# Kernel tuning notes

Measured on AMD Instinct MI355X. Metric: run time of the kernel, lower is better.

The kernel has to match this reference:

```python
import jax, jax.numpy as jnp
import numpy as np

B, C, H, W = 4, 64, 64, 64  # prompt and kv share the same BCHW shape
EPS = 1e-5
OFR = 4.0  # offset_range_factor
SCALE = (C // 1) ** -0.5  # n_head_channels = dim / n_heads = 64


def conv1x1(x, w, b=None):
    y = jnp.einsum('oc,bchw->bohw', w, x)
    if b is not None:
        y = y + b[None, :, None, None]
    return y


def grid_sample_bilinear(img, grid):
    # img: [N,C,Hp,Wp], grid: [N,Hg,Wg,2] with (x,y) in [-1,1], align_corners=True, zeros padding
    N, Cc, Hp, Wp = img.shape
    Hg, Wg = grid.shape[1], grid.shape[2]
    gx = (grid[..., 0] + 1.0) * 0.5 * (Wp - 1)
    gy = (grid[..., 1] + 1.0) * 0.5 * (Hp - 1)
    x0 = jnp.floor(gx)
    y0 = jnp.floor(gy)
    img_f = img.reshape(N, Cc, Hp * Wp)

    def gather(xi, yi):
        valid = (xi >= 0) & (xi <= Wp - 1) & (yi >= 0) & (yi <= Hp - 1)
        xi_c = jnp.clip(xi, 0, Wp - 1).astype(jnp.int32)
        yi_c = jnp.clip(yi, 0, Hp - 1).astype(jnp.int32)
        idx = (yi_c * Wp + xi_c).reshape(N, 1, -1)
        vals = jnp.take_along_axis(img_f, idx, axis=2)  # [N,C,Hg*Wg]
        return vals, valid.reshape(N, 1, -1).astype(img.dtype)

    v00, m00 = gather(x0, y0)
    v01, m01 = gather(x0 + 1, y0)
    v10, m10 = gather(x0, y0 + 1)
    v11, m11 = gather(x0 + 1, y0 + 1)
    wx = (gx - x0).reshape(N, 1, -1)
    wy = (gy - y0).reshape(N, 1, -1)
    out = (v00 * m00 * (1 - wx) * (1 - wy) + v01 * m01 * wx * (1 - wy)
           + v10 * m10 * (1 - wx) * wy + v11 * m11 * wx * wy)
    return out.reshape(N, Cc, Hg, Wg)


def setup_inputs() -> dict:
    key = jax.random.key(0)
    ks = jax.random.split(key, 8)
    s = 0.02
    return {
        'prompt': jax.random.normal(ks[0], (B, C, H, W), jnp.float32),
        'kv': jax.random.normal(ks[1], (B, C, H, W), jnp.float32),
        'wq': s * jax.random.normal(ks[2], (C, C), jnp.float32),
        'bq': jnp.zeros((C,), jnp.float32),
        'wk': s * jax.random.normal(ks[3], (C, C), jnp.float32),
        'bk': jnp.zeros((C,), jnp.float32),
        'wv': s * jax.random.normal(ks[4], (C, C), jnp.float32),
        'bv': jnp.zeros((C,), jnp.float32),
        'wo': s * jax.random.normal(ks[5], (C, C), jnp.float32),
        'bo': jnp.zeros((C,), jnp.float32),
        'dw_w': s * jax.random.normal(ks[6], (C, 1, 3, 3), jnp.float32),  # depthwise 3x3
        'dw_b': jnp.zeros((C,), jnp.float32),
        'ln_w': jnp.ones((C,), jnp.float32),
        'ln_b': jnp.zeros((C,), jnp.float32),
        'off_w': s * jax.random.normal(ks[7], (2, C), jnp.float32),  # 1x1 conv to 2 offset channels
    }


def reference(prompt, kv, wq, bq, wk, bk, wv, bv, wo, bo, dw_w, dw_b, ln_w, ln_b, off_w):
    # q projection (n_groups=1 so group view == full view)
    q = conv1x1(prompt, wq, bq)  # [B,C,H,W]

    # conv_offset: depthwise 3x3 -> WithBias LayerNorm over channels -> GELU -> 1x1 to 2ch
    t = jax.lax.conv_general_dilated(q, dw_w, (1, 1), ((1, 1), (1, 1)),
                                     feature_group_count=C)
    t = t + dw_b[None, :, None, None]
    mu = t.mean(axis=1, keepdims=True)
    var = t.var(axis=1, keepdims=True)
    t = (t - mu) / jnp.sqrt(var + EPS) * ln_w[None, :, None, None] + ln_b[None, :, None, None]
    t = jax.nn.gelu(t, approximate=False)
    offset = jnp.einsum('oc,bchw->bohw', off_w, t)  # [B,2,H,W] (y,x) channels

    Hk, Wk = offset.shape[2], offset.shape[3]
    n = Hk * Wk
    rng = jnp.array([1.0 / (Hk - 1.0), 1.0 / (Wk - 1.0)], dtype=offset.dtype).reshape(1, 2, 1, 1)
    offset = jnp.tanh(offset) * rng * OFR
    offset = jnp.transpose(offset, (0, 2, 3, 1))  # [B,Hk,Wk,2] (y,x)

    ref_y = (jnp.linspace(0.5, Hk - 0.5, Hk) / (Hk - 1.0)) * 2.0 - 1.0
    ref_x = (jnp.linspace(0.5, Wk - 0.5, Wk) / (Wk - 1.0)) * 2.0 - 1.0
    ry, rx = jnp.meshgrid(ref_y, ref_x, indexing='ij')
    ref = jnp.stack((ry, rx), axis=-1)[None].astype(offset.dtype)  # [1,Hk,Wk,2]

    pos = offset + ref
    grid = pos[..., ::-1]  # swap to (x,y)
    xs = grid_sample_bilinear(kv, grid)  # [B,C,Hk,Wk]
    xs = xs.reshape(B, C, n)

    k = jnp.einsum('oc,bcn->bon', wk, xs) + bk[None, :, None]
    v = jnp.einsum('oc,bcn->bon', wv, xs) + bv[None, :, None]
    qf = q.reshape(B, C, H * W)

    attn = jnp.einsum('bcm,bcn->bmn', qf, k) * SCALE  # [B,HW,n]
    attn = jax.nn.softmax(attn, axis=2)
    out = jnp.einsum('bmn,bcn->bcm', attn, v).reshape(B, C, H, W)
    return conv1x1(out, wo, bo)
```

## Files before the change

kernel.cpp:

```cpp
#include <hip/hip_runtime.h>
#include <math.h>

#define BB 4
#define CC 64
#define HH 64
#define WW 64
#define HWP 4096
#define NPTS 4096
#define LDP 72
constexpr float K_EPS   = 1e-5f;
constexpr float K_OFR   = 4.0f;
constexpr float K_QSCALE = 0.18033688011112042f;


typedef short frag8 __attribute__((ext_vector_type(8)));
typedef float f32x4 __attribute__((ext_vector_type(4)));

static __device__ inline unsigned short f2bf(float f) {
  unsigned int u = __builtin_bit_cast(unsigned int, f);
  unsigned int r = (u + 0x7fffu + ((u >> 16) & 1u)) >> 16;
  return (unsigned short)r;
}

__global__ __launch_bounds__(512) void k_qproj(
    const float* __restrict__ prompt, const float* __restrict__ wq,
    const float* __restrict__ bq, float* __restrict__ qf,
    unsigned short* __restrict__ qb) {
  __shared__ float w_s[64 * 64];
  __shared__ float p_s[64 * 64];
  __shared__ unsigned short t_s[64 * 68];
  int tid = threadIdx.x;
  int blk = blockIdx.x;
  int b = blk >> 6; int hw0 = (blk & 63) * 64;
#pragma unroll
  for (int i = 0; i < 8; ++i) w_s[i * 512 + tid] = wq[i * 512 + tid];
#pragma unroll
  for (int i = 0; i < 8; ++i) {
    int idx = i * 512 + tid; int c = idx >> 6, pix = idx & 63;
    p_s[idx] = prompt[(size_t)(b * CC + c) * HWP + hw0 + pix];
  }
  __syncthreads();
  int x = tid & 63, og = tid >> 6;
  float acc[8];
#pragma unroll
  for (int oo = 0; oo < 8; ++oo) acc[oo] = bq[og * 8 + oo];
  for (int cg = 0; cg < 16; ++cg) {
    float p0 = p_s[(cg * 4 + 0) * 64 + x];
    float p1 = p_s[(cg * 4 + 1) * 64 + x];
    float p2 = p_s[(cg * 4 + 2) * 64 + x];
    float p3 = p_s[(cg * 4 + 3) * 64 + x];
#pragma unroll
    for (int oo = 0; oo < 8; ++oo) {
      const float4 w4 = *(const float4*)&w_s[(og * 8 + oo) * 64 + cg * 4];
      acc[oo] = fmaf(w4.x, p0, fmaf(w4.y, p1, fmaf(w4.z, p2, fmaf(w4.w, p3, acc[oo]))));
    }
  }
#pragma unroll
  for (int oo = 0; oo < 8; ++oo) {
    int o = og * 8 + oo;
    qf[(size_t)(b * CC + o) * HWP + hw0 + x] = acc[oo];
    t_s[x * 68 + o] = f2bf(acc[oo] * K_QSCALE);
  }
  __syncthreads();
#pragma unroll
  for (int i = 0; i < 2; ++i) {
    int idx = i * 512 + tid;
    int pix = idx >> 4, c4 = idx & 15;
    ushort4 v = *(const ushort4*)&t_s[pix * 68 + c4 * 4];
    *(ushort4*)&qb[(size_t)(b * HWP + hw0 + pix) * CC + c4 * 4] = v;
  }
}

__global__ __launch_bounds__(512) void k_off_sample(
    const float* __restrict__ q, const float* __restrict__ dw_w,
    const float* __restrict__ dw_b, const float* __restrict__ ln_w,
    const float* __restrict__ ln_b, const float* __restrict__ off_w,
    const float* __restrict__ kv,
    const float* __restrict__ wk, const float* __restrict__ bk,
    const float* __restrict__ wv, const float* __restrict__ bv,
    unsigned short* __restrict__ kb, unsigned short* __restrict__ vb) {
  __shared__ float wk_s[64 * 64];
  __shared__ float wv_s[64 * 64];
  __shared__ float xs_s[64 * 64];
  __shared__ float red0[8][64];
  __shared__ float red1[8][64];

  int tid = threadIdx.x;
  int x = tid & 63;
  int cg = tid >> 6;
  int by = blockIdx.x;
  int b = by >> 6;
  int y = by & 63;

#pragma unroll
  for (int i = 0; i < 8; ++i) {
    wk_s[i * 512 + tid] = wk[i * 512 + tid];
    wv_s[i * 512 + tid] = wv[i * 512 + tid];
  }

  float t[8];
#pragma unroll
  for (int i = 0; i < 8; ++i) {
    int c = cg * 8 + i;
    float acc = dw_b[c];
    const float* qc = q + (size_t)(b * CC + c) * HWP;
#pragma unroll
    for (int ky = 0; ky < 3; ++ky) {
      int yy = y + ky - 1;
      bool yok = (yy >= 0) && (yy < HH);
#pragma unroll
      for (int kx = 0; kx < 3; ++kx) {
        int xx = x + kx - 1;
        bool ok = yok && (xx >= 0) && (xx < WW);
        float v = ok ? qc[yy * WW + xx] : 0.f;
        acc = fmaf(dw_w[c * 9 + ky * 3 + kx], v, acc);
      }
    }
    t[i] = acc;
  }
  float s1 = 0.f, s2 = 0.f;
#pragma unroll
  for (int i = 0; i < 8; ++i) { s1 += t[i]; s2 += t[i] * t[i]; }
  red0[cg][x] = s1;
  red1[cg][x] = s2;
  __syncthreads();
  float mu = 0.f, ms = 0.f;
#pragma unroll
  for (int g = 0; g < 8; ++g) { mu += red0[g][x]; ms += red1[g][x]; }
  mu *= (1.f / 64.f); ms *= (1.f / 64.f);
  float rstd = rsqrtf(ms - mu * mu + K_EPS);

  float oy = 0.f, ox = 0.f;
#pragma unroll
  for (int i = 0; i < 8; ++i) {
    int c = cg * 8 + i;
    float g = (t[i] - mu) * rstd * ln_w[c] + ln_b[c];
    g = 0.5f * g * (1.f + erff(g * 0.70710678118654752f));
    oy = fmaf(off_w[c], g, oy);
    ox = fmaf(off_w[CC + c], g, ox);
  }
  __syncthreads();
  red0[cg][x] = oy;
  red1[cg][x] = ox;
  __syncthreads();
  if (cg == 0) {
    float osy = 0.f, osx = 0.f;
#pragma unroll
    for (int g = 0; g < 8; ++g) { osy += red0[g][x]; osx += red1[g][x]; }
    osy = tanhf(osy) * (K_OFR / (HH - 1));
    osx = tanhf(osx) * (K_OFR / (WW - 1));
    float ry = (y + 0.5f) * (2.f / 63.f) - 1.f;
    float rx = (x + 0.5f) * (2.f / 63.f) - 1.f;
    red0[0][x] = (osx + rx + 1.f) * 0.5f * (WW - 1);
    red0[1][x] = (osy + ry + 1.f) * 0.5f * (HH - 1);
  }
  __syncthreads();

  int n = x, og = cg;
  int n0 = y * 64;
  float gx = red0[0][n], gy = red0[1][n];
  float x0f = floorf(gx), y0f = floorf(gy);
  float wx = gx - x0f, wy = gy - y0f;
  int x0 = (int)x0f, y0 = (int)y0f;
  int x1 = x0 + 1, y1 = y0 + 1;
  float m00 = (x0 >= 0 && x0 < WW && y0 >= 0 && y0 < HH) ? 1.f : 0.f;
  float m01 = (x1 >= 0 && x1 < WW && y0 >= 0 && y0 < HH) ? 1.f : 0.f;
  float m10 = (x0 >= 0 && x0 < WW && y1 >= 0 && y1 < HH) ? 1.f : 0.f;
  float m11 = (x1 >= 0 && x1 < WW && y1 >= 0 && y1 < HH) ? 1.f : 0.f;
  int x0c = min(max(x0, 0), WW - 1), x1c = min(max(x1, 0), WW - 1);
  int y0c = min(max(y0, 0), HH - 1), y1c = min(max(y1, 0), HH - 1);
  int i00 = y0c * WW + x0c, i01 = y0c * WW + x1c;
  int i10 = y1c * WW + x0c, i11 = y1c * WW + x1c;
  float w00 = m00 * (1.f - wx) * (1.f - wy);
  float w01 = m01 * wx * (1.f - wy);
  float w10 = m10 * (1.f - wx) * wy;
  float w11 = m11 * wx * wy;

  const float* base = kv + (size_t)b * CC * HWP;
#pragma unroll
  for (int i = 0; i < 8; ++i) {
    int c = og * 8 + i;
    const float* pc = base + (size_t)c * HWP;
    xs_s[c * 64 + n] = w00 * pc[i00] + w01 * pc[i01] + w10 * pc[i10] + w11 * pc[i11];
  }
  __syncthreads();
  float ak[8], av[8];
#pragma unroll
  for (int oo = 0; oo < 8; ++oo) { ak[oo] = bk[og * 8 + oo]; av[oo] = bv[og * 8 + oo]; }
  for (int cg2 = 0; cg2 < 16; ++cg2) {
    float p0 = xs_s[(cg2 * 4 + 0) * 64 + n];
    float p1 = xs_s[(cg2 * 4 + 1) * 64 + n];
    float p2 = xs_s[(cg2 * 4 + 2) * 64 + n];
    float p3 = xs_s[(cg2 * 4 + 3) * 64 + n];
#pragma unroll
    for (int oo = 0; oo < 8; ++oo) {
      int o = og * 8 + oo;
      const float4 k4 = *(const float4*)&wk_s[o * 64 + cg2 * 4];
      const float4 v4 = *(const float4*)&wv_s[o * 64 + cg2 * 4];
      ak[oo] = fmaf(k4.x, p0, fmaf(k4.y, p1, fmaf(k4.z, p2, fmaf(k4.w, p3, ak[oo]))));
      av[oo] = fmaf(v4.x, p0, fmaf(v4.y, p1, fmaf(v4.z, p2, fmaf(v4.w, p3, av[oo]))));
    }
  }
  unsigned short tk[8];
#pragma unroll
  for (int oo = 0; oo < 8; ++oo) tk[oo] = f2bf(ak[oo]);
  size_t krow = (size_t)(b * NPTS + n0 + n) * CC + og * 8;
  *(uint4*)&kb[krow] = *(const uint4*)&tk[0];
#pragma unroll
  for (int oo = 0; oo < 8; ++oo) {
    int o = og * 8 + oo;
    vb[(size_t)(b * CC + o) * NPTS + n0 + n] = f2bf(av[oo]);
  }
}

__global__ __launch_bounds__(256) void k_attn(
    const unsigned short* __restrict__ qb, const unsigned short* __restrict__ kb,
    const unsigned short* __restrict__ vb, float* __restrict__ opart,
    float* __restrict__ dpart, int ns_shift) {
  __shared__ short qp_s[64 * LDP];
  __shared__ short k_s[64 * LDP];
  __shared__ short v_s[64 * LDP];

  int tid = threadIdx.x;
  int w = tid >> 6, lane = tid & 63, quad = lane >> 4, l16 = lane & 15;
  int blk = blockIdx.x;
  int mt = blk & 63; int bns = blk >> 6;
  int ns = bns & ((1 << ns_shift) - 1); int b = bns >> ns_shift;
  int m0 = mt * 64;

  const unsigned short* qbb = qb + (size_t)b * HWP * CC;
  const unsigned short* kbb = kb + (size_t)b * NPTS * CC;
  const unsigned short* vbb = vb + (size_t)b * CC * NPTS;

#pragma unroll
  for (int pass = 0; pass < 2; ++pass) {
    int idx = pass * 256 + tid;
    int row = idx >> 3, part = idx & 7;
    uint4 d = *(const uint4*)(qbb + (size_t)(m0 + row) * CC + part * 8);
    *(uint4*)&qp_s[row * LDP + part * 8] = d;
  }
  __syncthreads();
  frag8 a_frag[2];
#pragma unroll
  for (int kc = 0; kc < 2; ++kc)
    a_frag[kc] = *(const frag8*)&qp_s[(w * 16 + l16) * LDP + kc * 32 + quad * 8];

  f32x4 o_acc[4];
  float d_acc[4];
#pragma unroll
  for (int i = 0; i < 4; ++i) {
    d_acc[i] = 0.f;
    o_acc[i][0] = 0.f; o_acc[i][1] = 0.f; o_acc[i][2] = 0.f; o_acc[i][3] = 0.f;
  }

  int niters = (NPTS / 64) >> ns_shift;
  int nbase = ns * niters * 64;
  for (int it = 0; it < niters; ++it) {
    int n0 = nbase + it * 64;
    __syncthreads();
#pragma unroll
    for (int pass = 0; pass < 2; ++pass) {
      int idx = pass * 256 + tid;
      int row = idx >> 3, part = idx & 7;
      uint4 dk = *(const uint4*)(kbb + (size_t)(n0 + row) * CC + part * 8);
      uint4 dv = *(const uint4*)(vbb + (size_t)row * NPTS + n0 + part * 8);
      *(uint4*)&k_s[row * LDP + part * 8] = dk;
      *(uint4*)&v_s[row * LDP + part * 8] = dv;
    }
    __syncthreads();

    f32x4 s_acc[4];
#pragma unroll
    for (int t = 0; t < 4; ++t) {
      s_acc[t][0] = 0.f; s_acc[t][1] = 0.f; s_acc[t][2] = 0.f; s_acc[t][3] = 0.f;
    }
#pragma unroll
    for (int kc = 0; kc < 2; ++kc) {
#pragma unroll
      for (int t = 0; t < 4; ++t) {
        frag8 bf = *(const frag8*)&k_s[(t * 16 + l16) * LDP + kc * 32 + quad * 8];
        s_acc[t] = __builtin_amdgcn_mfma_f32_16x16x32_bf16(a_frag[kc], bf, s_acc[t], 0, 0, 0);
      }
    }
#pragma unroll
    for (int t = 0; t < 4; ++t) {
#pragma unroll
      for (int r = 0; r < 4; ++r) {
        float pv = exp2f(s_acc[t][r]);
        unsigned short ph = f2bf(pv);
        qp_s[(w * 16 + quad * 4 + r) * LDP + t * 16 + l16] = (short)ph;
        d_acc[r] += __builtin_bit_cast(float, (unsigned int)ph << 16);
      }
    }
#pragma unroll
    for (int kc = 0; kc < 2; ++kc) {
      frag8 bp = *(const frag8*)&qp_s[(w * 16 + l16) * LDP + kc * 32 + quad * 8];
#pragma unroll
      for (int ct = 0; ct < 4; ++ct) {
        frag8 av = *(const frag8*)&v_s[(ct * 16 + l16) * LDP + kc * 32 + quad * 8];
        o_acc[ct] = __builtin_amdgcn_mfma_f32_16x16x32_bf16(av, bp, o_acc[ct], 0, 0, 0);
      }
    }
  }

  float* op = opart + (size_t)((ns * BB + b) * HWP + m0 + w * 16 + l16) * CC;
#pragma unroll
  for (int ct = 0; ct < 4; ++ct) {
    float4 o4;
    o4.x = o_acc[ct][0]; o4.y = o_acc[ct][1]; o4.z = o_acc[ct][2]; o4.w = o_acc[ct][3];
    *(float4*)&op[ct * 16 + quad * 4] = o4;
  }
#pragma unroll
  for (int r = 0; r < 4; ++r) {
    float d = d_acc[r];
    d += __shfl_xor(d, 1); d += __shfl_xor(d, 2);
    d += __shfl_xor(d, 4); d += __shfl_xor(d, 8);
    if (l16 == 0)
      dpart[(ns * BB + b) * HWP + m0 + w * 16 + quad * 4 + r] = d;
  }
}

__global__ __launch_bounds__(256) void k_out(
    const float* __restrict__ opart, const float* __restrict__ dpart,
    const float* __restrict__ wo, const float* __restrict__ bo,
    float* __restrict__ out, int NS) {
  __shared__ float wo_s[CC * CC];
  __shared__ float t_s[64 * 65];
  int tid = threadIdx.x;
  int blk = blockIdx.x;
  int b = blk >> 6, mt = blk & 63, m0 = mt * 64;
  for (int i = tid; i < CC * CC; i += 256) wo_s[i] = wo[i];

#pragma unroll
  for (int it = 0; it < 16; ++it) {
    int idx = it * 256 + tid;
    int m = idx >> 6, c = idx & 63;
    float o = 0.f, d = 0.f;
    for (int s = 0; s < NS; ++s) {
      o += opart[(size_t)((s * BB + b) * HWP + m0 + m) * CC + c];
      d += dpart[(s * BB + b) * HWP + m0 + m];
    }
    t_s[m * 65 + c] = o / d;
  }
  __syncthreads();
  int ml = tid & 63, og = tid >> 6;
  for (int oo = 0; oo < 16; ++oo) {
    int o = og * 16 + oo;
    float acc = bo[o];
#pragma unroll
    for (int c = 0; c < 64; ++c) acc = fmaf(wo_s[o * CC + c], t_s[ml * 65 + c], acc);
    out[(size_t)(b * CC + o) * HWP + m0 + ml] = acc;
  }
}

extern "C" void kernel_launch(void* const* d_in, const int* in_sizes, int n_in,
                              void* d_out, int out_size, void* d_ws, size_t ws_size,
                              hipStream_t stream) {
  const float* prompt = (const float*)d_in[0];
  const float* kv     = (const float*)d_in[1];
  const float* wq     = (const float*)d_in[2];
  const float* bq     = (const float*)d_in[3];
  const float* wk     = (const float*)d_in[4];
  const float* bk     = (const float*)d_in[5];
  const float* wv     = (const float*)d_in[6];
  const float* bv     = (const float*)d_in[7];
  const float* wo     = (const float*)d_in[8];
  const float* bo     = (const float*)d_in[9];
  const float* dw_w   = (const float*)d_in[10];
  const float* dw_b   = (const float*)d_in[11];
  const float* ln_w   = (const float*)d_in[12];
  const float* ln_b   = (const float*)d_in[13];
  const float* off_w  = (const float*)d_in[14];
  float* out = (float*)d_out;
  float* ws  = (float*)d_ws;

  const size_t need4 = (size_t)(4 * 1048576 + 3 * 524288 + 4 * 16384) * sizeof(float);
  int NS, ns_shift;
  if (ws_size >= need4) { NS = 4; ns_shift = 2; } else { NS = 2; ns_shift = 1; }

  float* opart          = ws;
  float* qf             = ws;
  unsigned short* qb    = (unsigned short*)(ws + (size_t)NS * 1048576);
  unsigned short* kb    = (unsigned short*)(ws + (size_t)NS * 1048576 + 524288);
  unsigned short* vb    = (unsigned short*)(ws + (size_t)NS * 1048576 + 2 * 524288);
  float* dpart          = ws + (size_t)NS * 1048576 + 3 * 524288;

  hipLaunchKernelGGL(k_qproj, dim3(BB * 64), dim3(512), 0, stream,
                     prompt, wq, bq, qf, qb);
  hipLaunchKernelGGL(k_off_sample, dim3(BB * HH), dim3(512), 0, stream,
                     qf, dw_w, dw_b, ln_w, ln_b, off_w,
                     kv, wk, bk, wv, bv, kb, vb);
  hipLaunchKernelGGL(k_attn, dim3(BB * NS * 64), dim3(256), 0, stream,
                     qb, kb, vb, opart, dpart, ns_shift);
  hipLaunchKernelGGL(k_out, dim3(BB * 64), dim3(256), 0, stream,
                     opart, dpart, wo, bo, out, NS);
}
```

Before: 177.7 us.

## Widen blocks, compute softmax denominator via MFMA, packed bf16 exp, more key splits

Several changes land at once. The projection and offset kernels move to 1024-thread blocks. The attention kernel computes S transposed so each lane holds contiguous columns, which it writes as packed bf16 pairs using native exp2 and pack conversion. The row-sum denominator now comes from an MFMA against a vector of ones instead of shuffle reductions. The key dimension is split into 8 when workspace allows, attention blocks are reordered so one query tile's key splits run adjacently, and the output kernel uses smaller tiles. Together these aim to raise parallelism and cut VALU and shuffle work, at the cost of more partial-sum traffic in the output kernel.

```diff
diff --git a/kernel.cpp b/kernel.cpp
--- a/kernel.cpp
+++ b/kernel.cpp
@@ -22,7 +22,28 @@
   return (unsigned short)r;
 }
 
-__global__ __launch_bounds__(512) void k_qproj(
+#if defined(__has_builtin)
+#if __has_builtin(__builtin_amdgcn_cvt_pk_bf16_f32)
+#define HAVE_CVT_PK_BF16 1
+#endif
+#if __has_builtin(__builtin_amdgcn_exp2f)
+#define EXP2F(x) __builtin_amdgcn_exp2f(x)
+#endif
+#endif
+#ifndef EXP2F
+#define EXP2F(x) exp2f(x)
+#endif
+
+static __device__ inline int pack2bf(float a, float b) {
+#ifdef HAVE_CVT_PK_BF16
+  auto r = __builtin_amdgcn_cvt_pk_bf16_f32(a, b);
+  return __builtin_bit_cast(int, r);
+#else
+  return (int)f2bf(a) | ((int)f2bf(b) << 16);
+#endif
+}
+
+__global__ __launch_bounds__(1024) void k_qproj(
     const float* __restrict__ prompt, const float* __restrict__ wq,
     const float* __restrict__ bq, float* __restrict__ qf,
     unsigned short* __restrict__ qb) {
@@ -33,45 +54,43 @@
   int blk = blockIdx.x;
   int b = blk >> 6; int hw0 = (blk & 63) * 64;
 #pragma unroll
-  for (int i = 0; i < 8; ++i) w_s[i * 512 + tid] = wq[i * 512 + tid];
-#pragma unroll
-  for (int i = 0; i < 8; ++i) {
-    int idx = i * 512 + tid; int c = idx >> 6, pix = idx & 63;
+  for (int i = 0; i < 4; ++i) w_s[i * 1024 + tid] = wq[i * 1024 + tid];
+#pragma unroll
+  for (int i = 0; i < 4; ++i) {
+    int idx = i * 1024 + tid; int c = idx >> 6, pix = idx & 63;
     p_s[idx] = prompt[(size_t)(b * CC + c) * HWP + hw0 + pix];
   }
   __syncthreads();
   int x = tid & 63, og = tid >> 6;
-  float acc[8];
-#pragma unroll
-  for (int oo = 0; oo < 8; ++oo) acc[oo] = bq[og * 8 + oo];
+  float acc[4];
+#pragma unroll
+  for (int oo = 0; oo < 4; ++oo) acc[oo] = bq[og * 4 + oo];
   for (int cg = 0; cg < 16; ++cg) {
     float p0 = p_s[(cg * 4 + 0) * 64 + x];
     float p1 = p_s[(cg * 4 + 1) * 64 + x];
     float p2 = p_s[(cg * 4 + 2) * 64 + x];
     float p3 = p_s[(cg * 4 + 3) * 64 + x];
 #pragma unroll
-    for (int oo = 0; oo < 8; ++oo) {
-      const float4 w4 = *(const float4*)&w_s[(og * 8 + oo) * 64 + cg * 4];
+    for (int oo = 0; oo < 4; ++oo) {
+      const float4 w4 = *(const float4*)&w_s[(og * 4 + oo) * 64 + cg * 4];
       acc[oo] = fmaf(w4.x, p0, fmaf(w4.y, p1, fmaf(w4.z, p2, fmaf(w4.w, p3, acc[oo]))));
     }
   }
 #pragma unroll
-  for (int oo = 0; oo < 8; ++oo) {
-    int o = og * 8 + oo;
+  for (int oo = 0; oo < 4; ++oo) {
+    int o = og * 4 + oo;
     qf[(size_t)(b * CC + o) * HWP + hw0 + x] = acc[oo];
     t_s[x * 68 + o] = f2bf(acc[oo] * K_QSCALE);
   }
   __syncthreads();
-#pragma unroll
-  for (int i = 0; i < 2; ++i) {
-    int idx = i * 512 + tid;
-    int pix = idx >> 4, c4 = idx & 15;
+  {
+    int pix = tid >> 4, c4 = tid & 15;
     ushort4 v = *(const ushort4*)&t_s[pix * 68 + c4 * 4];
     *(ushort4*)&qb[(size_t)(b * HWP + hw0 + pix) * CC + c4 * 4] = v;
   }
 }
 
-__global__ __launch_bounds__(512) void k_off_sample(
+__global__ __launch_bounds__(1024) void k_off_sample(
     const float* __restrict__ q, const float* __restrict__ dw_w,
     const float* __restrict__ dw_b, const float* __restrict__ ln_w,
     const float* __restrict__ ln_b, const float* __restrict__ off_w,
@@ -82,8 +101,8 @@
   __shared__ float wk_s[64 * 64];
   __shared__ float wv_s[64 * 64];
   __shared__ float xs_s[64 * 64];
-  __shared__ float red0[8][64];
-  __shared__ float red1[8][64];
+  __shared__ float red0[16][64];
+  __shared__ float red1[16][64];
 
   int tid = threadIdx.x;
   int x = tid & 63;
@@ -93,15 +112,15 @@
   int y = by & 63;
 
 #pragma unroll
-  for (int i = 0; i < 8; ++i) {
-    wk_s[i * 512 + tid] = wk[i * 512 + tid];
-    wv_s[i * 512 + tid] = wv[i * 512 + tid];
-  }
-
-  float t[8];
-#pragma unroll
-  for (int i = 0; i < 8; ++i) {
-    int c = cg * 8 + i;
+  for (int i = 0; i < 4; ++i) {
+    wk_s[i * 1024 + tid] = wk[i * 1024 + tid];
+    wv_s[i * 1024 + tid] = wv[i * 1024 + tid];
+  }
+
+  float t[4];
+#pragma unroll
+  for (int i = 0; i < 4; ++i) {
+    int c = cg * 4 + i;
     float acc = dw_b[c];
     const float* qc = q + (size_t)(b * CC + c) * HWP;
 #pragma unroll
@@ -120,20 +139,20 @@
   }
   float s1 = 0.f, s2 = 0.f;
 #pragma unroll
-  for (int i = 0; i < 8; ++i) { s1 += t[i]; s2 += t[i] * t[i]; }
+  for (int i = 0; i < 4; ++i) { s1 += t[i]; s2 += t[i] * t[i]; }
   red0[cg][x] = s1;
   red1[cg][x] = s2;
   __syncthreads();
   float mu = 0.f, ms = 0.f;
 #pragma unroll
-  for (int g = 0; g < 8; ++g) { mu += red0[g][x]; ms += red1[g][x]; }
+  for (int g = 0; g < 16; ++g) { mu += red0[g][x]; ms += red1[g][x]; }
   mu *= (1.f / 64.f); ms *= (1.f / 64.f);
   float rstd = rsqrtf(ms - mu * mu + K_EPS);
 
   float oy = 0.f, ox = 0.f;
 #pragma unroll
-  for (int i = 0; i < 8; ++i) {
-    int c = cg * 8 + i;
+  for (int i = 0; i < 4; ++i) {
+    int c = cg * 4 + i;
     float g = (t[i] - mu) * rstd * ln_w[c] + ln_b[c];
     g = 0.5f * g * (1.f + erff(g * 0.70710678118654752f));
     oy = fmaf(off_w[c], g, oy);
@@ -146,7 +165,7 @@
   if (cg == 0) {
     float osy = 0.f, osx = 0.f;
 #pragma unroll
-    for (int g = 0; g < 8; ++g) { osy += red0[g][x]; osx += red1[g][x]; }
+    for (int g = 0; g < 16; ++g) { osy += red0[g][x]; osx += red1[g][x]; }
     osy = tanhf(osy) * (K_OFR / (HH - 1));
     osx = tanhf(osx) * (K_OFR / (WW - 1));
     float ry = (y + 0.5f) * (2.f / 63.f) - 1.f;
@@ -178,37 +197,37 @@
 
   const float* base = kv + (size_t)b * CC * HWP;
 #pragma unroll
-  for (int i = 0; i < 8; ++i) {
-    int c = og * 8 + i;
+  for (int i = 0; i < 4; ++i) {
+    int c = og * 4 + i;
     const float* pc = base + (size_t)c * HWP;
     xs_s[c * 64 + n] = w00 * pc[i00] + w01 * pc[i01] + w10 * pc[i10] + w11 * pc[i11];
   }
   __syncthreads();
-  float ak[8], av[8];
-#pragma unroll
-  for (int oo = 0; oo < 8; ++oo) { ak[oo] = bk[og * 8 + oo]; av[oo] = bv[og * 8 + oo]; }
+  float ak[4], av[4];
+#pragma unroll
+  for (int oo = 0; oo < 4; ++oo) { ak[oo] = bk[og * 4 + oo]; av[oo] = bv[og * 4 + oo]; }
   for (int cg2 = 0; cg2 < 16; ++cg2) {
     float p0 = xs_s[(cg2 * 4 + 0) * 64 + n];
     float p1 = xs_s[(cg2 * 4 + 1) * 64 + n];
     float p2 = xs_s[(cg2 * 4 + 2) * 64 + n];
     float p3 = xs_s[(cg2 * 4 + 3) * 64 + n];
 #pragma unroll
-    for (int oo = 0; oo < 8; ++oo) {
-      int o = og * 8 + oo;
+    for (int oo = 0; oo < 4; ++oo) {
+      int o = og * 4 + oo;
       const float4 k4 = *(const float4*)&wk_s[o * 64 + cg2 * 4];
       const float4 v4 = *(const float4*)&wv_s[o * 64 + cg2 * 4];
       ak[oo] = fmaf(k4.x, p0, fmaf(k4.y, p1, fmaf(k4.z, p2, fmaf(k4.w, p3, ak[oo]))));
       av[oo] = fmaf(v4.x, p0, fmaf(v4.y, p1, fmaf(v4.z, p2, fmaf(v4.w, p3, av[oo]))));
     }
   }
-  unsigned short tk[8];
-#pragma unroll
-  for (int oo = 0; oo < 8; ++oo) tk[oo] = f2bf(ak[oo]);
-  size_t krow = (size_t)(b * NPTS + n0 + n) * CC + og * 8;
-  *(uint4*)&kb[krow] = *(const uint4*)&tk[0];
-#pragma unroll
-  for (int oo = 0; oo < 8; ++oo) {
-    int o = og * 8 + oo;
+  int2 kk;
+  kk.x = pack2bf(ak[0], ak[1]);
+  kk.y = pack2bf(ak[2], ak[3]);
+  size_t krow = (size_t)(b * NPTS + n0 + n) * CC + og * 4;
+  *(int2*)&kb[krow] = kk;
+#pragma unroll
+  for (int oo = 0; oo < 4; ++oo) {
+    int o = og * 4 + oo;
     vb[(size_t)(b * CC + o) * NPTS + n0 + n] = f2bf(av[oo]);
   }
 }
@@ -224,8 +243,10 @@
   int tid = threadIdx.x;
   int w = tid >> 6, lane = tid & 63, quad = lane >> 4, l16 = lane & 15;
   int blk = blockIdx.x;
-  int mt = blk & 63; int bns = blk >> 6;
-  int ns = bns & ((1 << ns_shift) - 1); int b = bns >> ns_shift;
+  int pair = blk & ((BB << ns_shift) - 1);
+  int mt = blk >> (2 + ns_shift);
+  int ns = pair & ((1 << ns_shift) - 1);
+  int b = pair >> ns_shift;
   int m0 = mt * 64;
 
   const unsigned short* qbb = qb + (size_t)b * HWP * CC;
@@ -245,13 +266,16 @@
   for (int kc = 0; kc < 2; ++kc)
     a_frag[kc] = *(const frag8*)&qp_s[(w * 16 + l16) * LDP + kc * 32 + quad * 8];
 
+  frag8 ones;
+#pragma unroll
+  for (int i = 0; i < 8; ++i) ones[i] = (short)0x3F80;
+
   f32x4 o_acc[4];
-  float d_acc[4];
-#pragma unroll
-  for (int i = 0; i < 4; ++i) {
-    d_acc[i] = 0.f;
-    o_acc[i][0] = 0.f; o_acc[i][1] = 0.f; o_acc[i][2] = 0.f; o_acc[i][3] = 0.f;
-  }
+  f32x4 d4;
+  const f32x4 zz = {0.f, 0.f, 0.f, 0.f};
+#pragma unroll
+  for (int i = 0; i < 4; ++i) o_acc[i] = zz;
+  d4 = zz;
 
   int niters = (NPTS / 64) >> ns_shift;
   int nbase = ns * niters * 64;
@@ -269,32 +293,29 @@
     }
     __syncthreads();
 
-    f32x4 s_acc[4];
+    f32x4 sT[4];
 #pragma unroll
     for (int t = 0; t < 4; ++t) {
-      s_acc[t][0] = 0.f; s_acc[t][1] = 0.f; s_acc[t][2] = 0.f; s_acc[t][3] = 0.f;
-    }
-#pragma unroll
-    for (int kc = 0; kc < 2; ++kc) {
-#pragma unroll
-      for (int t = 0; t < 4; ++t) {
-        frag8 bf = *(const frag8*)&k_s[(t * 16 + l16) * LDP + kc * 32 + quad * 8];
-        s_acc[t] = __builtin_amdgcn_mfma_f32_16x16x32_bf16(a_frag[kc], bf, s_acc[t], 0, 0, 0);
-      }
+      frag8 kf = *(const frag8*)&k_s[(t * 16 + l16) * LDP + quad * 8];
+      sT[t] = __builtin_amdgcn_mfma_f32_16x16x32_bf16(kf, a_frag[0], zz, 0, 0, 0);
     }
 #pragma unroll
     for (int t = 0; t < 4; ++t) {
-#pragma unroll
-      for (int r = 0; r < 4; ++r) {
-        float pv = exp2f(s_acc[t][r]);
-        unsigned short ph = f2bf(pv);
-        qp_s[(w * 16 + quad * 4 + r) * LDP + t * 16 + l16] = (short)ph;
-        d_acc[r] += __builtin_bit_cast(float, (unsigned int)ph << 16);
-      }
+      frag8 kf = *(const frag8*)&k_s[(t * 16 + l16) * LDP + 32 + quad * 8];
+      sT[t] = __builtin_amdgcn_mfma_f32_16x16x32_bf16(kf, a_frag[1], sT[t], 0, 0, 0);
+    }
+#pragma unroll
+    for (int t = 0; t < 4; ++t) {
+      int base_sh = (w * 16 + l16) * LDP + t * 16 + quad * 4;
+      int p01 = pack2bf(EXP2F(sT[t][0]), EXP2F(sT[t][1]));
+      int p23 = pack2bf(EXP2F(sT[t][2]), EXP2F(sT[t][3]));
+      *(int*)&qp_s[base_sh]     = p01;
+      *(int*)&qp_s[base_sh + 2] = p23;
     }
 #pragma unroll
     for (int kc = 0; kc < 2; ++kc) {
       frag8 bp = *(const frag8*)&qp_s[(w * 16 + l16) * LDP + kc * 32 + quad * 8];
+      d4 = __builtin_amdgcn_mfma_f32_16x16x32_bf16(ones, bp, d4, 0, 0, 0);
 #pragma unroll
       for (int ct = 0; ct < 4; ++ct) {
         frag8 av = *(const frag8*)&v_s[(ct * 16 + l16) * LDP + kc * 32 + quad * 8];
@@ -310,14 +331,8 @@
     o4.x = o_acc[ct][0]; o4.y = o_acc[ct][1]; o4.z = o_acc[ct][2]; o4.w = o_acc[ct][3];
     *(float4*)&op[ct * 16 + quad * 4] = o4;
   }
-#pragma unroll
-  for (int r = 0; r < 4; ++r) {
-    float d = d_acc[r];
-    d += __shfl_xor(d, 1); d += __shfl_xor(d, 2);
-    d += __shfl_xor(d, 4); d += __shfl_xor(d, 8);
-    if (l16 == 0)
-      dpart[(ns * BB + b) * HWP + m0 + w * 16 + quad * 4 + r] = d;
-  }
+  if (lane < 16)
+    dpart[(ns * BB + b) * HWP + m0 + w * 16 + lane] = d4[0];
 }
 
 __global__ __launch_bounds__(256) void k_out(
@@ -325,14 +340,14 @@
     const float* __restrict__ wo, const float* __restrict__ bo,
     float* __restrict__ out, int NS) {
   __shared__ float wo_s[CC * CC];
-  __shared__ float t_s[64 * 65];
+  __shared__ float t_s[32 * 65];
   int tid = threadIdx.x;
   int blk = blockIdx.x;
-  int b = blk >> 6, mt = blk & 63, m0 = mt * 64;
+  int b = blk >> 7, mt = blk & 127, m0 = mt * 32;
   for (int i = tid; i < CC * CC; i += 256) wo_s[i] = wo[i];
 
 #pragma unroll
-  for (int it = 0; it < 16; ++it) {
+  for (int it = 0; it < 8; ++it) {
     int idx = it * 256 + tid;
     int m = idx >> 6, c = idx & 63;
     float o = 0.f, d = 0.f;
@@ -343,9 +358,9 @@
     t_s[m * 65 + c] = o / d;
   }
   __syncthreads();
-  int ml = tid & 63, og = tid >> 6;
-  for (int oo = 0; oo < 16; ++oo) {
-    int o = og * 16 + oo;
+  int ml = tid & 31, og = tid >> 5;
+  for (int oo = 0; oo < 8; ++oo) {
+    int o = og * 8 + oo;
     float acc = bo[o];
 #pragma unroll
     for (int c = 0; c < 64; ++c) acc = fmaf(wo_s[o * CC + c], t_s[ml * 65 + c], acc);
@@ -374,9 +389,13 @@
   float* out = (float*)d_out;
   float* ws  = (float*)d_ws;
 
-  const size_t need4 = (size_t)(4 * 1048576 + 3 * 524288 + 4 * 16384) * sizeof(float);
+  auto need = [](int ns) {
+    return (size_t)((size_t)ns * 1048576 + 3 * 524288 + (size_t)ns * 16384) * sizeof(float);
+  };
   int NS, ns_shift;
-  if (ws_size >= need4) { NS = 4; ns_shift = 2; } else { NS = 2; ns_shift = 1; }
+  if      (ws_size >= need(8)) { NS = 8; ns_shift = 3; }
+  else if (ws_size >= need(4)) { NS = 4; ns_shift = 2; }
+  else                         { NS = 2; ns_shift = 1; }
 
   float* opart          = ws;
   float* qf             = ws;
@@ -385,13 +404,13 @@
   unsigned short* vb    = (unsigned short*)(ws + (size_t)NS * 1048576 + 2 * 524288);
   float* dpart          = ws + (size_t)NS * 1048576 + 3 * 524288;
 
-  hipLaunchKernelGGL(k_qproj, dim3(BB * 64), dim3(512), 0, stream,
+  hipLaunchKernelGGL(k_qproj, dim3(BB * 64), dim3(1024), 0, stream,
                      prompt, wq, bq, qf, qb);
-  hipLaunchKernelGGL(k_off_sample, dim3(BB * HH), dim3(512), 0, stream,
+  hipLaunchKernelGGL(k_off_sample, dim3(BB * HH), dim3(1024), 0, stream,
                      qf, dw_w, dw_b, ln_w, ln_b, off_w,
                      kv, wk, bk, wv, bv, kb, vb);
   hipLaunchKernelGGL(k_attn, dim3(BB * NS * 64), dim3(256), 0, stream,
                      qb, kb, vb, opart, dpart, ns_shift);
-  hipLaunchKernelGGL(k_out, dim3(BB * 64), dim3(256), 0, stream,
+  hipLaunchKernelGGL(k_out, dim3(BB * 128), dim3(256), 0, stream,
                      opart, dpart, wo, bo, out, NS);
 }
```

Result: faster. 168.8 us (-5.0%).
